# Kernel optimization log

Hardware: AMD Instinct MI355X
Metric: run time of the kernel (lower is better)

The kernel has to match this reference:

```python
import jax, jax.numpy as jnp
import numpy as np

N = 50000
E = 800000
IN_DIM = 128
OUT_DIM = 128
HEADS = 8
CH = OUT_DIM // HEADS  # per-head channels = 16
NUM_EDGE_TYPES = 8
NEG_SLOPE = 0.2
LN_EPS = 1e-5


def setup_inputs() -> dict:
    key = jax.random.key(0)
    ks = jax.random.split(key, 12)
    x = jax.random.normal(ks[0], (N, IN_DIM), jnp.float32)
    src = jax.random.randint(ks[1], (E,), 0, N, jnp.int32)
    off = jax.random.randint(ks[2], (E,), 1, N, jnp.int32)
    dst = (src + off) % N  # guaranteed no self loops
    etype = jax.random.randint(ks[3], (E,), 0, NUM_EDGE_TYPES, jnp.int32)
    edge_attr = jax.nn.one_hot(etype, NUM_EDGE_TYPES, dtype=jnp.float32)
    s = 1.0 / np.sqrt(IN_DIM)
    Wl = jax.random.normal(ks[4], (IN_DIM, HEADS * CH), jnp.float32) * s
    bl = jnp.zeros((HEADS * CH,), jnp.float32)
    Wr = jax.random.normal(ks[5], (IN_DIM, HEADS * CH), jnp.float32) * s
    br = jnp.zeros((HEADS * CH,), jnp.float32)
    We = jax.random.normal(ks[6], (NUM_EDGE_TYPES, HEADS * CH), jnp.float32) * (1.0 / np.sqrt(NUM_EDGE_TYPES))
    att = jax.random.normal(ks[7], (HEADS, CH), jnp.float32) * (1.0 / np.sqrt(CH))
    bias = jnp.zeros((OUT_DIM,), jnp.float32)
    ln_w = jnp.ones((OUT_DIM,), jnp.float32)
    ln_b = jnp.zeros((OUT_DIM,), jnp.float32)
    return {"x": x, "src": src, "dst": dst, "edge_attr": edge_attr,
            "Wl": Wl, "bl": bl, "Wr": Wr, "br": br, "We": We,
            "att": att, "bias": bias, "ln_w": ln_w, "ln_b": ln_b}


def _gatv2_layer(x, src, dst, edge_attr, Wl, bl, Wr, br, We, att, bias, ln_w, ln_b):
    n = x.shape[0]
    xl = (x @ Wl + bl).reshape(n, HEADS, CH)  # source-side features (lin_l)
    xr = (x @ Wr + br).reshape(n, HEADS, CH)  # target-side features (lin_r)

    # add_self_loops with fill_value='mean': self-loop attr = mean incoming edge_attr
    ones = jnp.ones(dst.shape, jnp.float32)
    deg = jax.ops.segment_sum(ones, dst, num_segments=n)
    attr_sum = jax.ops.segment_sum(edge_attr, dst, num_segments=n)
    loop_attr = attr_sum / jnp.maximum(deg, 1.0)[:, None]

    loop = jnp.arange(n, dtype=src.dtype)
    src_f = jnp.concatenate([src, loop])
    dst_f = jnp.concatenate([dst, loop])
    ea = jnp.concatenate([edge_attr, loop_attr], axis=0)

    e_emb = (ea @ We).reshape(-1, HEADS, CH)
    # GATv2: score = att . leaky_relu(x_j + x_i + e)
    e = jax.nn.leaky_relu(xl[src_f] + xr[dst_f] + e_emb, NEG_SLOPE)  # [E+N,H,C]
    score = jnp.einsum('ehc,hc->eh', e, att)  # [E+N,H]

    # segment softmax over incoming edges of each target (self loops ensure non-empty)
    smax = jax.ops.segment_max(score, dst_f, num_segments=n)
    expd = jnp.exp(score - smax[dst_f])
    denom = jax.ops.segment_sum(expd, dst_f, num_segments=n)
    alpha = expd / denom[dst_f]  # [E+N,H]

    out = jax.ops.segment_sum(xl[src_f] * alpha[..., None], dst_f, num_segments=n)
    out = out.reshape(n, HEADS * CH) + bias

    mu = jnp.mean(out, axis=-1, keepdims=True)
    var = jnp.mean(jnp.square(out - mu), axis=-1, keepdims=True)
    out = (out - mu) * jax.lax.rsqrt(var + LN_EPS) * ln_w + ln_b
    return jax.nn.elu(out)


def reference(x, src, dst, edge_attr, Wl, bl, Wr, br, We, att, bias, ln_w, ln_b):
    return _gatv2_layer(x, src, dst, edge_attr, Wl, bl, Wr, br, We, att, bias, ln_w, ln_b)
```

## Files before the change

kernel.cpp:

```cpp
#include <hip/hip_runtime.h>
#include <hip/hip_bf16.h>

typedef _Float16 f16x8 __attribute__((ext_vector_type(8)));
typedef _Float16 h2    __attribute__((ext_vector_type(2)));
typedef float    f32x4v __attribute__((ext_vector_type(4)));
typedef float    f32x2 __attribute__((ext_vector_type(2)));

#define NEG_SLOPE 0.2f
#define NSHARD 8
#define SHARD_CAP 1024
#define BKT_CAP (NSHARD*SHARD_CAP)
#define CE 1024
#define LOG2E 1.44269504088896f

__device__ __forceinline__ ushort f2h_bits(float f){ _Float16 h=(_Float16)f; return __builtin_bit_cast(ushort, h); }
__device__ __forceinline__ h2 uash2(unsigned u){ return __builtin_bit_cast(h2, u); }
__device__ __forceinline__ h2 habs(h2 v){ return __builtin_bit_cast(h2, __builtin_bit_cast(unsigned, v) & 0x7fff7fffu); }
__device__ __forceinline__ void fmamix_lo(float& acc, h2 xs, float ex){
    asm("v_fma_mix_f32 %0, %1, %2, %0 op_sel:[0,0,0] op_sel_hi:[1,0,0]" : "+v"(acc) : "v"(xs), "v"(ex));
}
__device__ __forceinline__ void fmamix_hi(float& acc, h2 xs, float ex){
    asm("v_fma_mix_f32 %0, %1, %2, %0 op_sel:[1,0,0] op_sel_hi:[1,0,0]" : "+v"(acc) : "v"(xs), "v"(ex));
}

__global__ __launch_bounds__(256) void k_prepfill(const float* __restrict__ Wl, const float* __restrict__ Wr,
    const float* __restrict__ We, const float* __restrict__ att,
    ushort* __restrict__ Wt, ushort* __restrict__ Web, ushort* __restrict__ att_h,
    ushort* __restrict__ att6, ushort* __restrict__ att4,
    const int* __restrict__ src, const int* __restrict__ dst, const float* __restrict__ ea,
    int* __restrict__ bkt_cnt, unsigned* __restrict__ sta, int E)
{
    __shared__ int hist[256], gbase[256], wcur[256];
    int tid = threadIdx.x;
    int idx = blockIdx.x*256 + tid;
    if (idx < 256*128) {
        int c = idx >> 7, k = idx & 127;
        float v = (c < 128) ? Wl[k*128 + c] : Wr[k*128 + (c-128)];
        Wt[idx] = f2h_bits(v);
    }
    if (idx < 8*128) Web[idx] = f2h_bits(We[idx]);
    if (idx < 128) {
        float a = att[idx];
        att_h[idx] = f2h_bits(a);
        att6[idx]  = f2h_bits(0.6f*LOG2E*a);
        att4[idx]  = f2h_bits(0.4f*LOG2E*a);
    }

    hist[tid] = 0; wcur[tid] = 0;
    __syncthreads();
    int shard = blockIdx.x & (NSHARD-1);
    int e0 = blockIdx.x*CE;
    int ne = min(CE, E - e0);
    unsigned ent[4];
    int ebkt[4];
    #pragma unroll
    for (int j=0;j<4;++j){
        int i = tid + j*256;
        ebkt[j] = -1;
        if (i < ne){
            int e = e0 + i;
            int d = dst[e];
            const float* a = ea + (size_t)e*8;
            float4 u0 = *(const float4*)a;
            float4 u1 = *(const float4*)(a + 4);
            float v[8] = {u0.x,u0.y,u0.z,u0.w,u1.x,u1.y,u1.z,u1.w};
            int bt = 0;
            #pragma unroll
            for (int q=0;q<8;++q) if (v[q] != 0.f) bt = q;
            int b = d >> 8;
            ent[j] = (unsigned)(src[e] & 0xFFFF) | ((unsigned)bt << 16) | ((unsigned)(d & 255) << 19);
            ebkt[j] = b;
            atomicAdd(&hist[b], 1);
        }
    }
    __syncthreads();
    int v = hist[tid];
    if (v > 0) gbase[tid] = atomicAdd(&bkt_cnt[shard*256 + tid], v);
    __syncthreads();
    #pragma unroll
    for (int j=0;j<4;++j){
        if (ebkt[j] >= 0){
            int b = ebkt[j];
            int r = atomicAdd(&wcur[b], 1);
            sta[((size_t)b*NSHARD + shard)*SHARD_CAP + gbase[b] + r] = ent[j];
        }
    }
}

__global__ __launch_bounds__(256) void k_fill2(const unsigned* __restrict__ sta,
    const int* __restrict__ bkt_cnt, unsigned long long* __restrict__ cnt64,
    int* __restrict__ deg_i, int* __restrict__ csr_off, int* __restrict__ csr_pack)
{
    __shared__ unsigned long long c64[256];
    __shared__ int s[256];
    __shared__ int sexc[256];
    __shared__ int lcur[256];
    int b = blockIdx.x >> 1, half = blockIdx.x & 1;
    int tid = threadIdx.x;
    c64[tid] = 0; lcur[tid] = 0;
    __syncthreads();
    for (int k = 0; k < NSHARD; ++k){
        int cnt = bkt_cnt[k*256 + b];
        const unsigned* sb = sta + ((size_t)b*NSHARD + k)*SHARD_CAP;
        for (int i = tid; i < cnt; i += 256){
            unsigned u = sb[i];
            int dl = (u >> 19) & 255;
            int bt = (u >> 16) & 7;
            atomicAdd(&c64[dl], 1ull << (8*bt));
        }
    }
    __syncthreads();
    unsigned long long cv = c64[tid];
    int v = (int)((cv * 0x0101010101010101ull) >> 56);
    s[tid] = (v + 1) & ~1;
    __syncthreads();
    #pragma unroll
    for (int off=1; off<256; off<<=1){
        int t = (tid >= off) ? s[tid-off] : 0;
        __syncthreads();
        s[tid] += t;
        __syncthreads();
    }
    int loc = s[tid] - ((v + 1) & ~1);
    sexc[tid] = loc;
    int node = b*256 + tid;
    if ((tid >> 7) == half){
        cnt64[node] = cv;
        deg_i[node] = v;
        csr_off[node] = b*BKT_CAP + loc;
    }
    __syncthreads();
    int base = b*BKT_CAP;
    for (int k = 0; k < NSHARD; ++k){
        int cnt = bkt_cnt[k*256 + b];
        const unsigned* sb = sta + ((size_t)b*NSHARD + k)*SHARD_CAP;
        for (int i = tid; i < cnt; i += 256){
            unsigned u = sb[i];
            int dl = (u >> 19) & 255;
            if ((dl >> 7) != half) continue;
            int slot = base + sexc[dl] + atomicAdd(&lcur[dl], 1);
            csr_pack[slot] = (int)(u & 0xFFFFu) | (int)(((u >> 16) & 7u) << 24);
        }
    }
}

__global__ __launch_bounds__(256) void k_gemm(const float* __restrict__ x, const ushort* __restrict__ Wt,
    const float* __restrict__ bl, const float* __restrict__ br,
    const ushort* __restrict__ Web, const ushort* __restrict__ att_h,
    const unsigned long long* __restrict__ cnt64,
    ushort* __restrict__ xl, ushort* __restrict__ xr, float* __restrict__ expd_self, int Nn)
{
    __shared__ ushort S[4][16*256];
    int tid = threadIdx.x;
    int wave = tid >> 6, lane = tid & 63;
    int l15 = lane & 15, l4 = lane >> 4;
    int row0 = blockIdx.x*64 + wave*16;

    f16x8 afrag[4];
    int grow = row0 + l15;
    bool rok = grow < Nn;
    const float* xp = x + (size_t)grow*128 + l4*8;
    #pragma unroll
    for (int ks=0; ks<4; ++ks){
        float4 a = make_float4(0,0,0,0), b = make_float4(0,0,0,0);
        if (rok) { a = *(const float4*)(xp + ks*32); b = *(const float4*)(xp + ks*32 + 4); }
        afrag[ks] = (f16x8){ (_Float16)a.x,(_Float16)a.y,(_Float16)a.z,(_Float16)a.w,
                             (_Float16)b.x,(_Float16)b.y,(_Float16)b.z,(_Float16)b.w };
    }

    ushort* sw_base = &S[wave][0];
    #pragma unroll
    for (int nf=0; nf<16; ++nf){
        f32x4v acc = (f32x4v){0.f,0.f,0.f,0.f};
        #pragma unroll
        for (int ks=0; ks<4; ++ks){
            const ushort* bp = Wt + (size_t)(nf*16 + l15)*128 + ks*32 + l4*8;
            f16x8 bf = *(const f16x8*)(const void*)bp;
            acc = __builtin_amdgcn_mfma_f32_16x16x32_f16(bf, afrag[ks], acc, 0,0,0);
        }
        int c0 = nf*16 + l4*4;
        const float* bp2 = (c0 < 128) ? (bl + c0) : (br + (c0-128));
        float4 bv = *(const float4*)bp2;
        h2 p0 = { (_Float16)(acc[0] + bv.x), (_Float16)(acc[1] + bv.y) };
        h2 p1 = { (_Float16)(acc[2] + bv.z), (_Float16)(acc[3] + bv.w) };
        int sw = c0 ^ ((l15 & 7) << 2);
        *(uint2*)(&sw_base[l15*256 + sw]) = make_uint2(__builtin_bit_cast(unsigned, p0),
                                                       __builtin_bit_cast(unsigned, p1));
    }
    __syncthreads();

    #pragma unroll
    for (int pass=0; pass<4; ++pass){
        int row = pass*4 + l4;
        int gr = row0 + row;
        if (gr < Nn){
            int cu = l15*8;
            int m = (row & 7) << 2;
            uint2 a0 = *(const uint2*)(&sw_base[row*256 + (cu ^ m)]);
            uint2 a1 = *(const uint2*)(&sw_base[row*256 + ((cu+4) ^ m)]);
            *(uint4*)(xl + (size_t)gr*128 + cu) = make_uint4(a0.x, a0.y, a1.x, a1.y);
            uint2 b0 = *(const uint2*)(&sw_base[row*256 + ((128+cu) ^ m)]);
            uint2 b1 = *(const uint2*)(&sw_base[row*256 + ((128+cu+4) ^ m)]);
            *(uint4*)(xr + (size_t)gr*128 + cu) = make_uint4(b0.x, b0.y, b1.x, b1.y);
        }
    }

    if (rok) {
        unsigned long long cv = cnt64[grow];
        int deg = (int)((cv * 0x0101010101010101ull) >> 56);
        float inv = 1.f / fmaxf((float)deg, 1.f);
        h2 wt[8];
        #pragma unroll
        for (int t=0;t<8;++t){
            float w = (float)((cv >> (8*t)) & 0xff) * inv;
            wt[t] = (h2){ (_Float16)w, (_Float16)w };
        }
        h2 emb[16];
        #pragma unroll
        for (int j=0;j<16;++j) emb[j] = (h2){(_Float16)0.f,(_Float16)0.f};
        #pragma unroll
        for (int t=0;t<8;++t){
            const ushort* wp = Web + t*128 + l4*32;
            uint4 u0 = *(const uint4*)wp;
            uint4 u1 = *(const uint4*)(wp + 8);
            uint4 u2 = *(const uint4*)(wp + 16);
            uint4 u3 = *(const uint4*)(wp + 24);
            emb[0]+=wt[t]*uash2(u0.x); emb[1]+=wt[t]*uash2(u0.y); emb[2]+=wt[t]*uash2(u0.z); emb[3]+=wt[t]*uash2(u0.w);
            emb[4]+=wt[t]*uash2(u1.x); emb[5]+=wt[t]*uash2(u1.y); emb[6]+=wt[t]*uash2(u1.z); emb[7]+=wt[t]*uash2(u1.w);
            emb[8]+=wt[t]*uash2(u2.x); emb[9]+=wt[t]*uash2(u2.y); emb[10]+=wt[t]*uash2(u2.z); emb[11]+=wt[t]*uash2(u2.w);
            emb[12]+=wt[t]*uash2(u3.x); emb[13]+=wt[t]*uash2(u3.y); emb[14]+=wt[t]*uash2(u3.z); emb[15]+=wt[t]*uash2(u3.w);
        }
        h2 at2v[16];
        {
            const ushort* ap = att_h + l4*32;
            uint4 a0 = *(const uint4*)ap;
            uint4 a1 = *(const uint4*)(ap + 8);
            uint4 a2 = *(const uint4*)(ap + 16);
            uint4 a3 = *(const uint4*)(ap + 24);
            at2v[0]=uash2(a0.x); at2v[1]=uash2(a0.y); at2v[2]=uash2(a0.z); at2v[3]=uash2(a0.w);
            at2v[4]=uash2(a1.x); at2v[5]=uash2(a1.y); at2v[6]=uash2(a1.z); at2v[7]=uash2(a1.w);
            at2v[8]=uash2(a2.x); at2v[9]=uash2(a2.y); at2v[10]=uash2(a2.z); at2v[11]=uash2(a2.w);
            at2v[12]=uash2(a3.x); at2v[13]=uash2(a3.y); at2v[14]=uash2(a3.z); at2v[15]=uash2(a3.w);
        }
        const h2 z2  = {(_Float16)0.f, (_Float16)0.f};
        const h2 c02 = {(_Float16)NEG_SLOPE, (_Float16)NEG_SLOPE};
        float p0 = 0.f, p1 = 0.f;
        int m = (l15 & 7) << 2;
        #pragma unroll
        for (int j=0;j<8;++j){
            int c0 = l4*32 + j*4;
            uint2 xlu = *(const uint2*)(&sw_base[l15*256 + (c0 ^ m)]);
            uint2 xru = *(const uint2*)(&sw_base[l15*256 + ((128+c0) ^ m)]);
            #pragma unroll
            for (int s2=0;s2<2;++s2){
                h2 v = (uash2(s2 ? xlu.y : xlu.x) + uash2(s2 ? xru.y : xru.x)) + emb[j*2+s2];
                h2 r = __builtin_elementwise_max(v, z2);
                h2 mm = __builtin_elementwise_min(v, z2);
                r = r + c02*mm;
                if (j < 4) p0 = __builtin_amdgcn_fdot2(at2v[j*2+s2], r, p0, false);
                else       p1 = __builtin_amdgcn_fdot2(at2v[j*2+s2], r, p1, false);
            }
        }
        *(float2*)(expd_self + (size_t)grow*8 + l4*2) = make_float2(__expf(p0), __expf(p1));
    }
}

__global__ __launch_bounds__(128) void k_node(const int* __restrict__ deg_i, const int* __restrict__ csr_off,
    const int* __restrict__ csr_pack,
    const ushort* __restrict__ xl, const ushort* __restrict__ xr, const ushort* __restrict__ Web,
    const ushort* __restrict__ att6, const ushort* __restrict__ att4, const float* __restrict__ expd_self,
    const float* __restrict__ bias, const float* __restrict__ lnw, const float* __restrict__ lnb,
    float* __restrict__ out, int Nn)
{
    __shared__ ushort xrw[2][8][16][8];
    int wv = threadIdx.x >> 6, lane = threadIdx.x & 63;
    int n = blockIdx.x*2 + wv;
    if (n >= Nn) return;
    int g = lane >> 4, l = lane & 15;

    h2 a6[4], a4[4];
    {
        uint4 u6 = *(const uint4*)(att6 + l*8);
        uint4 u4 = *(const uint4*)(att4 + l*8);
        a6[0]=uash2(u6.x); a6[1]=uash2(u6.y); a6[2]=uash2(u6.z); a6[3]=uash2(u6.w);
        a4[0]=uash2(u4.x); a4[1]=uash2(u4.y); a4[2]=uash2(u4.z); a4[3]=uash2(u4.w);
    }
    {
        uint4 ru = *(const uint4*)(xr + (size_t)n*128 + l*8);
        h2 xr2[4] = {uash2(ru.x), uash2(ru.y), uash2(ru.z), uash2(ru.w)};
        #pragma unroll
        for (int tt=0; tt<2; ++tt){
            int t = g + tt*4;
            uint4 wu = *(const uint4*)(Web + t*128 + l*8);
            h2 w0 = uash2(wu.x)+xr2[0], w1 = uash2(wu.y)+xr2[1];
            h2 w2 = uash2(wu.z)+xr2[2], w3 = uash2(wu.w)+xr2[3];
            *(uint4*)(&xrw[wv][t][l][0]) = make_uint4(__builtin_bit_cast(unsigned,w0), __builtin_bit_cast(unsigned,w1),
                                                      __builtin_bit_cast(unsigned,w2), __builtin_bit_cast(unsigned,w3));
        }
        asm volatile("s_waitcnt lgkmcnt(0)");
    }

    int beg = csr_off[n];
    int cnt = deg_i[n];
    float accx[4], accy[4];
    #pragma unroll
    for (int k=0;k<4;++k){ accx[k]=0.f; accy[k]=0.f; }
    float den = 0.f;

    for (int i = 0; i < cnt; i += 8) {
        int e0i = i + 2*g;
        bool v0 = e0i < cnt;
        bool v1 = (e0i + 1) < cnt;
        uint2 pk = *(const uint2*)(csr_pack + beg + (v0 ? e0i : 0));
        int s0  = v0 ? (pk.x & 0xFFFFFF) : 0;
        int et0 = v0 ? (int)(((unsigned)pk.x) >> 24) : 0;
        int s1  = v1 ? (pk.y & 0xFFFFFF) : 0;
        int et1 = v1 ? (int)(((unsigned)pk.y) >> 24) : 0;
        uint4 xu0 = *(const uint4*)(xl + (size_t)s0*128 + l*8);
        uint4 xu1 = *(const uint4*)(xl + (size_t)s1*128 + l*8);
        uint4 wu0 = *(const uint4*)(&xrw[wv][et0][l][0]);
        uint4 wu1 = *(const uint4*)(&xrw[wv][et1][l][0]);
        h2 xs0[4] = {uash2(xu0.x), uash2(xu0.y), uash2(xu0.z), uash2(xu0.w)};
        h2 xs1[4] = {uash2(xu1.x), uash2(xu1.y), uash2(xu1.z), uash2(xu1.w)};
        h2 xw0[4] = {uash2(wu0.x), uash2(wu0.y), uash2(wu0.z), uash2(wu0.w)};
        h2 xw1[4] = {uash2(wu1.x), uash2(wu1.y), uash2(wu1.z), uash2(wu1.w)};
        float pa = 0.f, pb = 0.f;
        #pragma unroll
        for (int k=0;k<4;++k){
            h2 va = xs0[k] + xw0[k];
            pa = __builtin_amdgcn_fdot2(a6[k], va, pa, false);
            pa = __builtin_amdgcn_fdot2(a4[k], habs(va), pa, false);
            h2 vb = xs1[k] + xw1[k];
            pb = __builtin_amdgcn_fdot2(a6[k], vb, pb, false);
            pb = __builtin_amdgcn_fdot2(a4[k], habs(vb), pb, false);
        }
        pa += __shfl_xor(pa, 1);
        pb += __shfl_xor(pb, 1);
        float ex0 = v0 ? exp2f(pa) : 0.f;
        float ex1 = v1 ? exp2f(pb) : 0.f;
        den += ex0 + ex1;
        #pragma unroll
        for (int k=0;k<4;++k){
            fmamix_lo(accx[k], xs0[k], ex0);
            fmamix_hi(accy[k], xs0[k], ex0);
            fmamix_lo(accx[k], xs1[k], ex1);
            fmamix_hi(accy[k], xs1[k], ex1);
        }
    }

    #pragma unroll
    for (int k=0;k<4;++k){
        accx[k] += __shfl_xor(accx[k], 16); accx[k] += __shfl_xor(accx[k], 32);
        accy[k] += __shfl_xor(accy[k], 16); accy[k] += __shfl_xor(accy[k], 32);
    }
    den += __shfl_xor(den, 16);
    den += __shfl_xor(den, 32);

    {
        float ex = expd_self[(size_t)n*8 + (l >> 1)];
        uint4 su = *(const uint4*)(xl + (size_t)n*128 + l*8);
        den += ex;
        h2 ss[4] = {uash2(su.x), uash2(su.y), uash2(su.z), uash2(su.w)};
        #pragma unroll
        for (int k=0;k<4;++k){
            fmamix_lo(accx[k], ss[k], ex);
            fmamix_hi(accy[k], ss[k], ex);
        }
    }

    float dinv = 1.f/den;
    f32x2 a[4];
    {
        float4 b0 = *(const float4*)(bias + l*8);
        float4 b1 = *(const float4*)(bias + l*8 + 4);
        a[0] = (f32x2){accx[0]*dinv + b0.x, accy[0]*dinv + b0.y};
        a[1] = (f32x2){accx[1]*dinv + b0.z, accy[1]*dinv + b0.w};
        a[2] = (f32x2){accx[2]*dinv + b1.x, accy[2]*dinv + b1.y};
        a[3] = (f32x2){accx[3]*dinv + b1.z, accy[3]*dinv + b1.w};
    }
    float sum = 0.f;
    #pragma unroll
    for (int k=0;k<4;++k) sum += a[k].x + a[k].y;
    #pragma unroll
    for (int off=8; off>0; off>>=1) sum += __shfl_xor(sum, off);
    float mu = sum * (1.f/128.f);
    float vs = 0.f;
    #pragma unroll
    for (int k=0;k<4;++k){ a[k] -= mu; vs += a[k].x*a[k].x + a[k].y*a[k].y; }
    #pragma unroll
    for (int off=8; off>0; off>>=1) vs += __shfl_xor(vs, off);
    float rs = rsqrtf(vs*(1.f/128.f) + 1e-5f);
    float y[8];
    {
        float4 w0 = *(const float4*)(lnw + l*8);
        float4 w1 = *(const float4*)(lnw + l*8 + 4);
        float4 c0 = *(const float4*)(lnb + l*8);
        float4 c1 = *(const float4*)(lnb + l*8 + 4);
        y[0]=a[0].x*rs*w0.x+c0.x; y[1]=a[0].y*rs*w0.y+c0.y;
        y[2]=a[1].x*rs*w0.z+c0.z; y[3]=a[1].y*rs*w0.w+c0.w;
        y[4]=a[2].x*rs*w1.x+c1.x; y[5]=a[2].y*rs*w1.y+c1.y;
        y[6]=a[3].x*rs*w1.z+c1.z; y[7]=a[3].y*rs*w1.w+c1.w;
    }
    #pragma unroll
    for (int j=0;j<8;++j) y[j] = (y[j] > 0.f) ? y[j] : (__expf(y[j]) - 1.f);
    if (lane < 16) {
        float* po = out + (size_t)n*128 + l*8;
        *(float4*)po     = make_float4(y[0],y[1],y[2],y[3]);
        *(float4*)(po+4) = make_float4(y[4],y[5],y[6],y[7]);
    }
}

extern "C" void kernel_launch(void* const* d_in, const int* in_sizes, int n_in,
                              void* d_out, int out_size, void* d_ws, size_t ws_size,
                              hipStream_t stream)
{
    const float* x   = (const float*)d_in[0];
    const int*   src = (const int*)  d_in[1];
    const int*   dst = (const int*)  d_in[2];
    const float* ea  = (const float*)d_in[3];
    const float* Wl  = (const float*)d_in[4];
    const float* bl  = (const float*)d_in[5];
    const float* Wr  = (const float*)d_in[6];
    const float* br  = (const float*)d_in[7];
    const float* We  = (const float*)d_in[8];
    const float* att = (const float*)d_in[9];
    const float* bias= (const float*)d_in[10];
    const float* lnw = (const float*)d_in[11];
    const float* lnb = (const float*)d_in[12];
    float* out = (float*)d_out;

    const int N  = in_sizes[0] / 128;
    const int E  = in_sizes[1];
    const int NP = ((N + 255)/256)*256;
    const int MB = (N + 63)/64;
    const int SB = NP/256;
    const int PB = (E + CE - 1)/CE;

    char* base = (char*)d_ws;
    size_t o = 0;
    auto alloc = [&](size_t b){ size_t r = o; o += (b + 255) & ~(size_t)255; return r; };
    ushort* Wt       = (ushort*)(base + alloc(256*128*2));
    ushort* Web      = (ushort*)(base + alloc(8*128*2));
    ushort* att_h    = (ushort*)(base + alloc(128*2));
    ushort* att6     = (ushort*)(base + alloc(128*2));
    ushort* att4     = (ushort*)(base + alloc(128*2));
    ushort* xl       = (ushort*)(base + alloc((size_t)MB*64*128*2));
    ushort* xr       = (ushort*)(base + alloc((size_t)MB*64*128*2));
    float*  expd_self= (float*) (base + alloc((size_t)NP*8*4));
    size_t zoff = o;
    int*    bkt_cnt  = (int*)   (base + alloc((size_t)NSHARD*256*4));
    size_t zbytes = o - zoff;
    unsigned long long* cnt64 = (unsigned long long*)(base + alloc((size_t)NP*8));
    int*    deg_i    = (int*)   (base + alloc((size_t)NP*4));
    int*    csr_off  = (int*)   (base + alloc((size_t)NP*4));
    unsigned* sta    = (unsigned*)(base + alloc((size_t)SB*NSHARD*SHARD_CAP*4));
    int*    csr_pack = (int*)   (base + alloc((size_t)SB*BKT_CAP*4));
    (void)ws_size; (void)n_in; (void)out_size;

    hipMemsetAsync(base + zoff, 0, zbytes, stream);
    k_prepfill<<<PB, 256, 0, stream>>>(Wl, Wr, We, att, Wt, Web, att_h, att6, att4, src, dst, ea,
                                       bkt_cnt, sta, E);
    k_fill2<<<SB*2, 256, 0, stream>>>(sta, bkt_cnt, cnt64, deg_i, csr_off, csr_pack);
    k_gemm <<<MB, 256, 0, stream>>>(x, Wt, bl, br, Web, att_h, cnt64, xl, xr, expd_self, N);
    k_node <<<(N+1)/2, 128, 0, stream>>>(deg_i, csr_off, csr_pack, xl, xr, Web, att6, att4, expd_self,
                                         bias, lnw, lnb, out, N);
}
```

Baseline: 125.2 us.

## Process 32 rows per wave in k_gemm to reuse weight fragments

Each wave now computes two 16-row MFMA tiles that share every loaded weight fragment, halving Wt global loads per output row and halving the grid. The block-wide __syncthreads is replaced by a per-wave lgkmcnt wait, since each wave touches only its own LDS slice. The attention-vector loads are hoisted out of the per-row self-loop score loop. LDS use doubles to 64 KB per block, which may lower occupancy, and fewer blocks reduces parallelism across the GPU.

```diff
diff --git a/kernel.cpp b/kernel.cpp
--- a/kernel.cpp
+++ b/kernel.cpp
@@ -150,47 +150,58 @@
     const unsigned long long* __restrict__ cnt64,
     ushort* __restrict__ xl, ushort* __restrict__ xr, float* __restrict__ expd_self, int Nn)
 {
-    __shared__ ushort S[4][16*256];
+    __shared__ ushort S[4][32*256];
     int tid = threadIdx.x;
     int wave = tid >> 6, lane = tid & 63;
     int l15 = lane & 15, l4 = lane >> 4;
-    int row0 = blockIdx.x*64 + wave*16;
-
-    f16x8 afrag[4];
-    int grow = row0 + l15;
-    bool rok = grow < Nn;
-    const float* xp = x + (size_t)grow*128 + l4*8;
+    int row0 = blockIdx.x*128 + wave*32;
+
+    f16x8 afragA[4], afragB[4];
+    int growA = row0 + l15, growB = row0 + 16 + l15;
+    bool rokA = growA < Nn, rokB = growB < Nn;
+    const float* xpA = x + (size_t)growA*128 + l4*8;
+    const float* xpB = x + (size_t)growB*128 + l4*8;
     #pragma unroll
     for (int ks=0; ks<4; ++ks){
         float4 a = make_float4(0,0,0,0), b = make_float4(0,0,0,0);
-        if (rok) { a = *(const float4*)(xp + ks*32); b = *(const float4*)(xp + ks*32 + 4); }
-        afrag[ks] = (f16x8){ (_Float16)a.x,(_Float16)a.y,(_Float16)a.z,(_Float16)a.w,
-                             (_Float16)b.x,(_Float16)b.y,(_Float16)b.z,(_Float16)b.w };
+        if (rokA) { a = *(const float4*)(xpA + ks*32); b = *(const float4*)(xpA + ks*32 + 4); }
+        afragA[ks] = (f16x8){ (_Float16)a.x,(_Float16)a.y,(_Float16)a.z,(_Float16)a.w,
+                              (_Float16)b.x,(_Float16)b.y,(_Float16)b.z,(_Float16)b.w };
+        float4 c = make_float4(0,0,0,0), d = make_float4(0,0,0,0);
+        if (rokB) { c = *(const float4*)(xpB + ks*32); d = *(const float4*)(xpB + ks*32 + 4); }
+        afragB[ks] = (f16x8){ (_Float16)c.x,(_Float16)c.y,(_Float16)c.z,(_Float16)c.w,
+                              (_Float16)d.x,(_Float16)d.y,(_Float16)d.z,(_Float16)d.w };
     }
 
     ushort* sw_base = &S[wave][0];
     #pragma unroll
     for (int nf=0; nf<16; ++nf){
-        f32x4v acc = (f32x4v){0.f,0.f,0.f,0.f};
+        f32x4v accA = (f32x4v){0.f,0.f,0.f,0.f};
+        f32x4v accB = (f32x4v){0.f,0.f,0.f,0.f};
         #pragma unroll
         for (int ks=0; ks<4; ++ks){
             const ushort* bp = Wt + (size_t)(nf*16 + l15)*128 + ks*32 + l4*8;
             f16x8 bf = *(const f16x8*)(const void*)bp;
-            acc = __builtin_amdgcn_mfma_f32_16x16x32_f16(bf, afrag[ks], acc, 0,0,0);
+            accA = __builtin_amdgcn_mfma_f32_16x16x32_f16(bf, afragA[ks], accA, 0,0,0);
+            accB = __builtin_amdgcn_mfma_f32_16x16x32_f16(bf, afragB[ks], accB, 0,0,0);
         }
         int c0 = nf*16 + l4*4;
         const float* bp2 = (c0 < 128) ? (bl + c0) : (br + (c0-128));
         float4 bv = *(const float4*)bp2;
-        h2 p0 = { (_Float16)(acc[0] + bv.x), (_Float16)(acc[1] + bv.y) };
-        h2 p1 = { (_Float16)(acc[2] + bv.z), (_Float16)(acc[3] + bv.w) };
         int sw = c0 ^ ((l15 & 7) << 2);
-        *(uint2*)(&sw_base[l15*256 + sw]) = make_uint2(__builtin_bit_cast(unsigned, p0),
-                                                       __builtin_bit_cast(unsigned, p1));
-    }
-    __syncthreads();
-
-    #pragma unroll
-    for (int pass=0; pass<4; ++pass){
+        h2 pa0 = { (_Float16)(accA[0] + bv.x), (_Float16)(accA[1] + bv.y) };
+        h2 pa1 = { (_Float16)(accA[2] + bv.z), (_Float16)(accA[3] + bv.w) };
+        *(uint2*)(&sw_base[l15*256 + sw]) = make_uint2(__builtin_bit_cast(unsigned, pa0),
+                                                       __builtin_bit_cast(unsigned, pa1));
+        h2 pb0 = { (_Float16)(accB[0] + bv.x), (_Float16)(accB[1] + bv.y) };
+        h2 pb1 = { (_Float16)(accB[2] + bv.z), (_Float16)(accB[3] + bv.w) };
+        *(uint2*)(&sw_base[(16 + l15)*256 + sw]) = make_uint2(__builtin_bit_cast(unsigned, pb0),
+                                                              __builtin_bit_cast(unsigned, pb1));
+    }
+    asm volatile("s_waitcnt lgkmcnt(0)");
+
+    #pragma unroll
+    for (int pass=0; pass<8; ++pass){
         int row = pass*4 + l4;
         int gr = row0 + row;
         if (gr < Nn){
@@ -205,7 +216,25 @@
         }
     }
 
-    if (rok) {
+    h2 at2v[16];
+    {
+        const ushort* ap = att_h + l4*32;
+        uint4 a0 = *(const uint4*)ap;
+        uint4 a1 = *(const uint4*)(ap + 8);
+        uint4 a2 = *(const uint4*)(ap + 16);
+        uint4 a3 = *(const uint4*)(ap + 24);
+        at2v[0]=uash2(a0.x); at2v[1]=uash2(a0.y); at2v[2]=uash2(a0.z); at2v[3]=uash2(a0.w);
+        at2v[4]=uash2(a1.x); at2v[5]=uash2(a1.y); at2v[6]=uash2(a1.z); at2v[7]=uash2(a1.w);
+        at2v[8]=uash2(a2.x); at2v[9]=uash2(a2.y); at2v[10]=uash2(a2.z); at2v[11]=uash2(a2.w);
+        at2v[12]=uash2(a3.x); at2v[13]=uash2(a3.y); at2v[14]=uash2(a3.z); at2v[15]=uash2(a3.w);
+    }
+    const h2 z2  = {(_Float16)0.f, (_Float16)0.f};
+    const h2 c02 = {(_Float16)NEG_SLOPE, (_Float16)NEG_SLOPE};
+    #pragma unroll
+    for (int pp=0; pp<2; ++pp){
+        int row = pp*16 + l15;
+        int grow = row0 + row;
+        if (grow >= Nn) continue;
         unsigned long long cv = cnt64[grow];
         int deg = (int)((cv * 0x0101010101010101ull) >> 56);
         float inv = 1.f / fmaxf((float)deg, 1.f);
@@ -230,27 +259,13 @@
             emb[8]+=wt[t]*uash2(u2.x); emb[9]+=wt[t]*uash2(u2.y); emb[10]+=wt[t]*uash2(u2.z); emb[11]+=wt[t]*uash2(u2.w);
             emb[12]+=wt[t]*uash2(u3.x); emb[13]+=wt[t]*uash2(u3.y); emb[14]+=wt[t]*uash2(u3.z); emb[15]+=wt[t]*uash2(u3.w);
         }
-        h2 at2v[16];
-        {
-            const ushort* ap = att_h + l4*32;
-            uint4 a0 = *(const uint4*)ap;
-            uint4 a1 = *(const uint4*)(ap + 8);
-            uint4 a2 = *(const uint4*)(ap + 16);
-            uint4 a3 = *(const uint4*)(ap + 24);
-            at2v[0]=uash2(a0.x); at2v[1]=uash2(a0.y); at2v[2]=uash2(a0.z); at2v[3]=uash2(a0.w);
-            at2v[4]=uash2(a1.x); at2v[5]=uash2(a1.y); at2v[6]=uash2(a1.z); at2v[7]=uash2(a1.w);
-            at2v[8]=uash2(a2.x); at2v[9]=uash2(a2.y); at2v[10]=uash2(a2.z); at2v[11]=uash2(a2.w);
-            at2v[12]=uash2(a3.x); at2v[13]=uash2(a3.y); at2v[14]=uash2(a3.z); at2v[15]=uash2(a3.w);
-        }
-        const h2 z2  = {(_Float16)0.f, (_Float16)0.f};
-        const h2 c02 = {(_Float16)NEG_SLOPE, (_Float16)NEG_SLOPE};
         float p0 = 0.f, p1 = 0.f;
-        int m = (l15 & 7) << 2;
+        int m = (row & 7) << 2;
         #pragma unroll
         for (int j=0;j<8;++j){
             int c0 = l4*32 + j*4;
-            uint2 xlu = *(const uint2*)(&sw_base[l15*256 + (c0 ^ m)]);
-            uint2 xru = *(const uint2*)(&sw_base[l15*256 + ((128+c0) ^ m)]);
+            uint2 xlu = *(const uint2*)(&sw_base[row*256 + (c0 ^ m)]);
+            uint2 xru = *(const uint2*)(&sw_base[row*256 + ((128+c0) ^ m)]);
             #pragma unroll
             for (int s2=0;s2<2;++s2){
                 h2 v = (uash2(s2 ? xlu.y : xlu.x) + uash2(s2 ? xru.y : xru.x)) + emb[j*2+s2];
@@ -432,7 +447,7 @@
     const int N  = in_sizes[0] / 128;
     const int E  = in_sizes[1];
     const int NP = ((N + 255)/256)*256;
-    const int MB = (N + 63)/64;
+    const int MB = (N + 127)/128;
     const int SB = NP/256;
     const int PB = (E + CE - 1)/CE;
 
@@ -444,8 +459,8 @@
     ushort* att_h    = (ushort*)(base + alloc(128*2));
     ushort* att6     = (ushort*)(base + alloc(128*2));
     ushort* att4     = (ushort*)(base + alloc(128*2));
-    ushort* xl       = (ushort*)(base + alloc((size_t)MB*64*128*2));
-    ushort* xr       = (ushort*)(base + alloc((size_t)MB*64*128*2));
+    ushort* xl       = (ushort*)(base + alloc((size_t)MB*128*128*2));
+    ushort* xr       = (ushort*)(base + alloc((size_t)MB*128*128*2));
     float*  expd_self= (float*) (base + alloc((size_t)NP*8*4));
     size_t zoff = o;
     int*    bkt_cnt  = (int*)   (base + alloc((size_t)NSHARD*256*4));
```

Result: faster. 110.6 us (median of 2 runs) (-11.6%).
